# Performance work log

Hardware: AMD Instinct MI355X
Metric: run time of the kernel (lower is better)

## Reference

```python
import jax, jax.numpy as jnp
import numpy as np

N_FEAT = 350; D = 512; L = 4; DS = 64; NREG = 6; REG_E = 32
B = 32; S = 2048
CLAMP = 20.0


def _ln(x, g, b, eps=1e-5):
    mu = jnp.mean(x, axis=-1, keepdims=True)
    var = jnp.mean(jnp.square(x - mu), axis=-1, keepdims=True)
    return (x - mu) * jax.lax.rsqrt(var + eps) * g + b


def _slstm(x, ln_g, ln_b, Wi, bi, Wf, bf, Wz, bz, Wo, bo, Wp, bp):
    # x: [B,S,D] -> out: [B,S,D]
    xn = _ln(x, ln_g, ln_b)
    log_i = jnp.clip(jnp.einsum('bsd,de->bse', xn, Wi) + bi, -CLAMP, CLAMP)
    log_f = jnp.clip(jnp.einsum('bsd,de->bse', xn, Wf) + bf, -CLAMP, CLAMP)
    z = jnp.tanh(jnp.einsum('bsd,de->bse', xn, Wz) + bz)
    o = jax.nn.sigmoid(jnp.einsum('bsd,de->bse', xn, Wo) + bo)

    def step(carry, inp):
        m, c = carry
        li, lf, zt, ot = inp
        m_new = jnp.maximum(m + lf, li)
        i_s = jnp.exp(li - m_new)
        f_s = jnp.exp(m + lf - m_new)
        c_new = f_s * c + i_s * zt
        h = ot * jnp.tanh(c_new)
        return (m_new, c_new), h

    bsz = x.shape[0]
    init = (jnp.zeros((bsz, DS), x.dtype), jnp.zeros((bsz, DS), x.dtype))
    seq = (jnp.swapaxes(log_i, 0, 1), jnp.swapaxes(log_f, 0, 1),
           jnp.swapaxes(z, 0, 1), jnp.swapaxes(o, 0, 1))
    _, hs = jax.lax.scan(step, init, seq)  # hs: [S,B,DS]
    hs = jnp.swapaxes(hs, 0, 1)  # [B,S,DS]
    return jnp.einsum('bse,ed->bsd', hs, Wp) + bp


def setup_inputs() -> dict:
    key = jax.random.key(0)
    ks = iter(jax.random.split(key, 64))
    def p(*shape):
        return jax.random.normal(next(ks), shape, dtype=jnp.float32) * 0.02
    return {
        'x': jax.random.normal(next(ks), (B, S, N_FEAT), dtype=jnp.float32),
        'regime_ids': jax.random.randint(next(ks), (B, S), 0, NREG),
        'emb_regime': p(NREG, REG_E),
        'grn_w1': p(N_FEAT + REG_E, D), 'grn_b1': jnp.zeros((D,), jnp.float32),
        'grn_w2': p(D, N_FEAT), 'grn_b2': jnp.zeros((N_FEAT,), jnp.float32),
        'in_w': p(N_FEAT, D), 'in_b': jnp.zeros((D,), jnp.float32),
        'ln_in_g': jnp.ones((L, D), jnp.float32), 'ln_in_b': jnp.zeros((L, D), jnp.float32),
        'wi': p(L, D, DS), 'bi': jnp.zeros((L, DS), jnp.float32),
        'wf': p(L, D, DS), 'bf': jnp.zeros((L, DS), jnp.float32),
        'wz': p(L, D, DS), 'bz': jnp.zeros((L, DS), jnp.float32),
        'wo': p(L, D, DS), 'bo': jnp.zeros((L, DS), jnp.float32),
        'wp': p(L, DS, D), 'bp': jnp.zeros((L, D), jnp.float32),
        'nm_g': jnp.ones((L, D), jnp.float32), 'nm_b': jnp.zeros((L, D), jnp.float32),
        'hd15_w': p(D, 1), 'hd15_b': jnp.zeros((1,), jnp.float32),
        'hd30_w': p(D, 1), 'hd30_b': jnp.zeros((1,), jnp.float32),
        'hv_w': p(D, 3), 'hv_b': jnp.zeros((3,), jnp.float32),
        'hreg_w': p(D, NREG), 'hreg_b': jnp.zeros((NREG,), jnp.float32),
        'hrng_w': p(D, 3), 'hrng_b': jnp.zeros((3,), jnp.float32),
    }


def reference(x, regime_ids, emb_regime, grn_w1, grn_b1, grn_w2, grn_b2,
              in_w, in_b, ln_in_g, ln_in_b, wi, bi, wf, bf, wz, bz, wo, bo,
              wp, bp, nm_g, nm_b, hd15_w, hd15_b, hd30_w, hd30_b,
              hv_w, hv_b, hreg_w, hreg_b, hrng_w, hrng_b):
    # Variable selection network (regime-conditioned feature weights)
    remb = emb_regime[regime_ids]                      # [B,S,32]
    comb = jnp.concatenate([x, remb], axis=-1)         # [B,S,382]
    hidden = jax.nn.elu(jnp.einsum('bsf,fd->bsd', comb, grn_w1) + grn_b1)
    weights = jax.nn.softmax(jnp.einsum('bsd,df->bsf', hidden, grn_w2) + grn_b2, axis=-1)
    xw = x * weights
    h = jnp.einsum('bsf,fd->bsd', xw, in_w) + in_b     # [B,S,D]
    for l in range(L):
        res = _slstm(h, ln_in_g[l], ln_in_b[l], wi[l], bi[l], wf[l], bf[l],
                     wz[l], bz[l], wo[l], bo[l], wp[l], bp[l])
        h = _ln(h + res, nm_g[l], nm_b[l])
    h_last = h[:, -1, :]
    return (jnp.squeeze(h_last @ hd15_w + hd15_b, -1),
            jnp.squeeze(h_last @ hd30_w + hd30_b, -1),
            h_last @ hv_w + hv_b,
            h_last @ hreg_w + hreg_b,
            h_last @ hrng_w + hrng_b,
            h_last,
            weights[:, -1, :])
```

## Files before the change

kernel.cpp:

```cpp
#include <hip/hip_runtime.h>
#include <cmath>

#define NFEAT 350
#define DMODEL 512
#define NLAYER 4
#define DSZ 64
#define REG_E 32
#define BATCH 32
#define SEQ 2048
#define MTOK (BATCH * SEQ)
#define CLAMP_V 20.0f

#define CHUNK 64
#define NCHUNK (SEQ / CHUNK)

typedef short bf16x8 __attribute__((ext_vector_type(8)));
typedef float f32x4 __attribute__((ext_vector_type(4)));

__device__ __forceinline__ unsigned short f2b(float v) {
    union { float f; unsigned int u; } x; x.f = v;
    unsigned int r = x.u + 0x7fffu + ((x.u >> 16) & 1u);
    return (unsigned short)(r >> 16);
}
__device__ __forceinline__ float b2f(unsigned short u) {
    union { unsigned int i; float f; } x; x.i = ((unsigned int)u) << 16;
    return x.f;
}
__device__ __forceinline__ unsigned int pack2(float a, float b) {
    return ((unsigned int)f2b(b) << 16) | f2b(a);
}

__global__ __launch_bounds__(256) void tconv_k(const float* __restrict__ src,
                                               unsigned short* __restrict__ dst,
                                               int K, int N, int Kpad) {
    int k = blockIdx.x * 256 + threadIdx.x;
    int n = blockIdx.y;
    if (k >= Kpad) return;
    float v = (k < K && n < N) ? src[(size_t)k * N + n] : 0.f;
    dst[(size_t)n * Kpad + k] = f2b(v);
}

__global__ __launch_bounds__(256) void tconv_wp_k(const float* __restrict__ wp,
                                                  unsigned short* __restrict__ dst) {
    int idx = blockIdx.x * 256 + threadIdx.x;
    int l = idx >> 15;
    int rem = idx & 32767;
    int n = rem >> 6;
    int k = rem & 63;
    float v = wp[((size_t)l * 64 + k) * 512 + n];
    unsigned short hi = f2b(v);
    unsigned short lo = f2b(v - b2f(hi));
    unsigned short* d = dst + ((size_t)l * 512 + n) * 128;
    d[k] = hi;
    d[64 + k] = lo;
}

__global__ __launch_bounds__(256) void tconv_g_k(const float* __restrict__ wi,
                                                 const float* __restrict__ wf,
                                                 const float* __restrict__ wz,
                                                 const float* __restrict__ wo,
                                                 unsigned short* __restrict__ dst) {
    int k = blockIdx.x * 256 + threadIdx.x;
    int n = blockIdx.y;
    int z = blockIdx.z;
    int l = z >> 2, g = z & 3;
    const float* src = (g == 0 ? wi : g == 1 ? wf : g == 2 ? wz : wo) + (size_t)l * DMODEL * DSZ;
    dst[(size_t)z * 32768 + (size_t)n * 512 + k] = f2b(src[(size_t)k * DSZ + n]);
}

__global__ __launch_bounds__(1024) void gbias_k(const float* bi, const float* bf_,
                                                const float* bz, const float* bo,
                                                float* __restrict__ gbias) {
    int t = threadIdx.x;
    int l = t >> 8, r = t & 255, g = r >> 6, e = r & 63;
    const float* s = (g == 0 ? bi : g == 1 ? bf_ : g == 2 ? bz : bo);
    gbias[t] = s[l * 64 + e];
}

__global__ __launch_bounds__(256) void build_xc_k(const float* __restrict__ x,
                                                  const int* __restrict__ rid,
                                                  const float* __restrict__ emb,
                                                  unsigned short* __restrict__ xc) {
    int i = blockIdx.x * 256 + threadIdx.x;
    int m = i / 192, p = i - m * 192;
    int k = p * 2;
    float a = 0.f, b = 0.f;
    if (k < 350) {
        const float2 v = *(const float2*)(x + (size_t)m * NFEAT + k);
        a = v.x; b = v.y;
    } else if (k < 382) {
        int r = rid[m];
        const float2 v = *(const float2*)(emb + r * REG_E + (k - 350));
        a = v.x; b = v.y;
    }
    ((unsigned int*)xc)[(size_t)m * 192 + p] = pack2(a, b);
}

template <int ALD, int EPI>
__global__ __launch_bounds__(256) void mgemm_k(const unsigned short* __restrict__ Ab,
                                               const float* __restrict__ Af,
                                               const unsigned short* __restrict__ Bt,
                                               const float* __restrict__ bias,
                                               float* __restrict__ Cf,
                                               unsigned short* __restrict__ Cb,
                                               const float* __restrict__ muA,
                                               const float* __restrict__ rstdA,
                                               const float* __restrict__ lng,
                                               const float* __restrict__ lnb,
                                               int lda, int ldb, int K, int N, int ldc) {
    __shared__ unsigned short As[128][40];
    __shared__ unsigned short Bs[128][40];
    const int tid = threadIdx.x;
    const int lane = tid & 63;
    const int wave = tid >> 6;
    const int l15 = lane & 15;
    const int quad = lane >> 4;
    const int wm = (wave >> 1) * 64;
    const int wn = (wave & 1) * 64;
    const size_t m0 = (size_t)blockIdx.y * 128;
    const int n0 = blockIdx.x * 128;

    const int sr = tid >> 2;
    const int ku = tid & 3;

    const unsigned short* Br0 = Bt + ((size_t)(n0 + sr)) * ldb + ku * 8;
    const unsigned short* Br1 = Br0 + (size_t)64 * ldb;

    const unsigned short* Ar0 = nullptr;
    const unsigned short* Ar1 = nullptr;
    const float* Fr0 = nullptr;
    const float* Fr1 = nullptr;
    float mu0 = 0.f, rs0 = 0.f, mu1 = 0.f, rs1 = 0.f;
    if (ALD == 0) {
        Ar0 = Ab + (m0 + sr) * (size_t)lda + ku * 8;
        Ar1 = Ar0 + (size_t)64 * lda;
    } else {
        Fr0 = Af + (m0 + sr) * (size_t)lda + ku * 8;
        Fr1 = Fr0 + (size_t)64 * lda;
        mu0 = muA[m0 + sr];   rs0 = rstdA[m0 + sr];
        mu1 = muA[m0 + sr + 64]; rs1 = rstdA[m0 + sr + 64];
    }

    f32x4 acc[4][4] = {};

    for (int k0 = 0; k0 < K; k0 += 32) {
        if (ALD == 0) {
            *(uint4*)&As[sr][ku * 8]      = *(const uint4*)(Ar0 + k0);
            *(uint4*)&As[sr + 64][ku * 8] = *(const uint4*)(Ar1 + k0);
        } else {
            float4 g0 = *(const float4*)(lng + k0 + ku * 8);
            float4 g1 = *(const float4*)(lng + k0 + ku * 8 + 4);
            float4 c0 = *(const float4*)(lnb + k0 + ku * 8);
            float4 c1 = *(const float4*)(lnb + k0 + ku * 8 + 4);
            {
                float4 v0 = *(const float4*)(Fr0 + k0);
                float4 v1 = *(const float4*)(Fr0 + k0 + 4);
                uint4 w;
                w.x = pack2((v0.x - mu0) * rs0 * g0.x + c0.x, (v0.y - mu0) * rs0 * g0.y + c0.y);
                w.y = pack2((v0.z - mu0) * rs0 * g0.z + c0.z, (v0.w - mu0) * rs0 * g0.w + c0.w);
                w.z = pack2((v1.x - mu0) * rs0 * g1.x + c1.x, (v1.y - mu0) * rs0 * g1.y + c1.y);
                w.w = pack2((v1.z - mu0) * rs0 * g1.z + c1.z, (v1.w - mu0) * rs0 * g1.w + c1.w);
                *(uint4*)&As[sr][ku * 8] = w;
            }
            {
                float4 v0 = *(const float4*)(Fr1 + k0);
                float4 v1 = *(const float4*)(Fr1 + k0 + 4);
                uint4 w;
                w.x = pack2((v0.x - mu1) * rs1 * g0.x + c0.x, (v0.y - mu1) * rs1 * g0.y + c0.y);
                w.y = pack2((v0.z - mu1) * rs1 * g0.z + c0.z, (v0.w - mu1) * rs1 * g0.w + c0.w);
                w.z = pack2((v1.x - mu1) * rs1 * g1.x + c1.x, (v1.y - mu1) * rs1 * g1.y + c1.y);
                w.w = pack2((v1.z - mu1) * rs1 * g1.z + c1.z, (v1.w - mu1) * rs1 * g1.w + c1.w);
                *(uint4*)&As[sr + 64][ku * 8] = w;
            }
        }
        *(uint4*)&Bs[sr][ku * 8]      = *(const uint4*)(Br0 + k0);
        *(uint4*)&Bs[sr + 64][ku * 8] = *(const uint4*)(Br1 + k0);
        __syncthreads();
        bf16x8 af[4], bf[4];
#pragma unroll
        for (int mt = 0; mt < 4; mt++)
            af[mt] = *(const bf16x8*)&As[wm + mt * 16 + l15][quad * 8];
#pragma unroll
        for (int nt = 0; nt < 4; nt++)
            bf[nt] = *(const bf16x8*)&Bs[wn + nt * 16 + l15][quad * 8];
#pragma unroll
        for (int mt = 0; mt < 4; mt++)
#pragma unroll
            for (int nt = 0; nt < 4; nt++)
                acc[mt][nt] = __builtin_amdgcn_mfma_f32_16x16x32_bf16(af[mt], bf[nt], acc[mt][nt], 0, 0, 0);
        __syncthreads();
    }

#pragma unroll
    for (int mt = 0; mt < 4; mt++) {
        int gmb = wm + mt * 16 + quad * 4;
#pragma unroll
        for (int nt = 0; nt < 4; nt++) {
            int gn = n0 + wn + nt * 16 + l15;
            if (gn < N) {
                float bv = bias[gn];
#pragma unroll
                for (int r = 0; r < 4; r++) {
                    size_t gm = m0 + gmb + r;
                    float v = acc[mt][nt][r] + bv;
                    if (EPI == 0) {
                        v = v > 0.f ? v : expm1f(v);
                        Cb[gm * (size_t)ldc + gn] = f2b(v);
                    } else if (EPI == 1) {
                        Cb[gm * (size_t)ldc + gn] = f2b(v);
                    } else if (EPI == 2) {
                        int g = gn >> 6;
                        if (g < 2) v = fminf(fmaxf(v, -CLAMP_V), CLAMP_V);
                        else if (g == 2) v = tanhf(v);
                        else v = 1.f / (1.f + expf(-v));
                        Cf[gm * (size_t)ldc + gn] = v;
                    } else {
                        Cf[gm * (size_t)ldc + gn] = v;
                    }
                }
            }
        }
    }
}

__global__ __launch_bounds__(256) void softmax_xw_k(const unsigned short* __restrict__ logits,
                                                    unsigned short* __restrict__ xc,
                                                    float* __restrict__ out_wlast) {
    int tok = blockIdx.x * 4 + (threadIdx.x >> 6);
    int lane = threadIdx.x & 63;
    const unsigned short* lr = logits + (size_t)tok * NFEAT;
    unsigned short* xr = xc + (size_t)tok * 384;
    float v[6];
    float mx = -1e30f;
#pragma unroll
    for (int i = 0; i < 6; i++) {
        int idx = lane + 64 * i;
        v[i] = (idx < NFEAT) ? b2f(lr[idx]) : -1e30f;
        mx = fmaxf(mx, v[i]);
    }
#pragma unroll
    for (int o = 32; o > 0; o >>= 1) mx = fmaxf(mx, __shfl_xor(mx, o, 64));
    float s = 0.f;
#pragma unroll
    for (int i = 0; i < 6; i++) { v[i] = expf(v[i] - mx); s += v[i]; }
#pragma unroll
    for (int o = 32; o > 0; o >>= 1) s += __shfl_xor(s, o, 64);
    float inv = 1.f / s;
    bool last = ((tok & (SEQ - 1)) == SEQ - 1);
    int b = tok >> 11;
#pragma unroll
    for (int i = 0; i < 6; i++) {
        int idx = lane + 64 * i;
        if (idx < NFEAT) {
            float w = v[i] * inv;
            xr[idx] = f2b(w * b2f(xr[idx]));
            if (last) out_wlast[b * NFEAT + idx] = w;
        } else if (idx < 352) {
            xr[idx] = 0;
        }
    }
}

__global__ __launch_bounds__(256) void ln_stats_k(const float* __restrict__ h,
                                                  float* __restrict__ mu,
                                                  float* __restrict__ rstd) {
    int tok = blockIdx.x * 4 + (threadIdx.x >> 6);
    int lane = threadIdx.x & 63;
    const float* row = h + (size_t)tok * DMODEL;
    float s = 0.f, sq = 0.f;
#pragma unroll
    for (int i = 0; i < 8; i++) {
        float v = row[lane + 64 * i];
        s += v;
        sq += v * v;
    }
#pragma unroll
    for (int o = 32; o > 0; o >>= 1) {
        s += __shfl_xor(s, o, 64);
        sq += __shfl_xor(sq, o, 64);
    }
    if (lane == 0) {
        float m = s * (1.f / DMODEL);
        float var = sq * (1.f / DMODEL) - m * m;
        mu[tok] = m;
        rstd[tok] = rsqrtf(var + 1e-5f);
    }
}

__global__ __launch_bounds__(256) void seg_agg_k(const float* __restrict__ gates,
                                                 float* __restrict__ aggF,
                                                 float* __restrict__ aggL,
                                                 float* __restrict__ aggS) {
    int b = blockIdx.x >> 3;
    int cg = blockIdx.x & 7;
    int chunk = cg * 4 + (threadIdx.x >> 6);
    int e = threadIdx.x & 63;
    const float* gp = gates + ((size_t)b * SEQ + (size_t)chunk * CHUNK) * 256;
    float F = 0.f, L = -1e30f, s = 0.f;
#pragma unroll 4
    for (int t = 0; t < CHUNK; t++) {
        const float* q = gp + (size_t)t * 256;
        float li = q[e], lf = q[64 + e], z = q[128 + e];
        float Ln = fmaxf(L + lf, li);
        s = expf(L + lf - Ln) * s + expf(li - Ln) * z;
        L = Ln;
        F += lf;
    }
    int idx = (b * NCHUNK + chunk) * 64 + e;
    aggF[idx] = F; aggL[idx] = L; aggS[idx] = s;
}

__global__ __launch_bounds__(64) void chunk_scan_k(const float* __restrict__ aggF,
                                                   const float* __restrict__ aggL,
                                                   const float* __restrict__ aggS,
                                                   float* __restrict__ stM,
                                                   float* __restrict__ stC) {
    int b = blockIdx.x;
    int e = threadIdx.x;
    float m = 0.f, c = 0.f;
    for (int k = 0; k < NCHUNK; k++) {
        int idx = (b * NCHUNK + k) * 64 + e;
        stM[idx] = m; stC[idx] = c;
        float F = aggF[idx], L = aggL[idx], s = aggS[idx];
        float mn = fmaxf(m + F, L);
        c = expf(m + F - mn) * c + expf(L - mn) * s;
        m = mn;
    }
}

__global__ __launch_bounds__(256) void replay_k(const float* __restrict__ gates,
                                                const float* __restrict__ stM,
                                                const float* __restrict__ stC,
                                                unsigned short* __restrict__ hs) {
    int b = blockIdx.x >> 3;
    int cg = blockIdx.x & 7;
    int chunk = cg * 4 + (threadIdx.x >> 6);
    int e = threadIdx.x & 63;
    int s0 = chunk * CHUNK;
    const float* gp = gates + ((size_t)b * SEQ + s0) * 256;
    unsigned short* hp = hs + ((size_t)b * SEQ + s0) * 128;
    int idx = (b * NCHUNK + chunk) * 64 + e;
    float m = stM[idx], c = stC[idx];
#pragma unroll 4
    for (int t = 0; t < CHUNK; t++) {
        const float* q = gp + (size_t)t * 256;
        float li = q[e], lf = q[64 + e], z = q[128 + e], o = q[192 + e];
        float mlf = m + lf;
        float mn = fmaxf(mlf, li);
        c = expf(mlf - mn) * c + expf(li - mn) * z;
        m = mn;
        float v = o * tanhf(c);
        unsigned short hi = f2b(v);
        hp[(size_t)t * 128 + e] = hi;
        hp[(size_t)t * 128 + 64 + e] = f2b(v - b2f(hi));
    }
}

__global__ __launch_bounds__(512) void outproj_mfma_k(const unsigned short* __restrict__ hs,
                                                      const unsigned short* __restrict__ wpt,
                                                      const float* __restrict__ bp,
                                                      const float* __restrict__ nmg,
                                                      const float* __restrict__ nmb,
                                                      float* __restrict__ h,
                                                      float* __restrict__ mu,
                                                      float* __restrict__ rstd) {
    __shared__ unsigned short As[32][136];
    __shared__ float sS[32][4], sQ[32][4];
    __shared__ float sS2[32][4], sQ2[32][4];
    const int tid = threadIdx.x;
    const int lane = tid & 63;
    const int wave = tid >> 6;
    const int l15 = lane & 15;
    const int quad = lane >> 4;
    const int wm = (wave >> 2) * 16;
    const int wn = (wave & 3) * 128;
    const int cg = wave & 3;
    const size_t tok0 = (size_t)blockIdx.x * 32;

    {
        int row = tid >> 4, ku = tid & 15;
        *(uint4*)&As[row][ku * 8] = *(const uint4*)(hs + (tok0 + row) * 128 + ku * 8);
    }
    __syncthreads();

    f32x4 acc[8] = {};
#pragma unroll 1
    for (int term = 0; term < 3; term++) {
        const int aoff = (term == 2) ? 64 : 0;
        const int boff = (term == 1) ? 64 : 0;
#pragma unroll
        for (int ks = 0; ks < 2; ks++) {
            bf16x8 af = *(const bf16x8*)&As[wm + l15][aoff + ks * 32 + quad * 8];
#pragma unroll
            for (int nt = 0; nt < 8; nt++) {
                bf16x8 bv = *(const bf16x8*)(wpt + (size_t)(wn + nt * 16 + l15) * 128 + boff + ks * 32 + quad * 8);
                acc[nt] = __builtin_amdgcn_mfma_f32_16x16x32_bf16(af, bv, acc[nt], 0, 0, 0);
            }
        }
    }

    float bpv[8], gv[8], bv_[8];
#pragma unroll
    for (int nt = 0; nt < 8; nt++) {
        int col = wn + nt * 16 + l15;
        bpv[nt] = bp[col]; gv[nt] = nmg[col]; bv_[nt] = nmb[col];
    }

#pragma unroll
    for (int r = 0; r < 4; r++) {
        int trow = wm + quad * 4 + r;
        const float* hrow = h + (tok0 + trow) * (size_t)DMODEL;
        float s = 0.f, sq = 0.f;
#pragma unroll
        for (int nt = 0; nt < 8; nt++) {
            float u = acc[nt][r] + bpv[nt] + hrow[wn + nt * 16 + l15];
            acc[nt][r] = u;
            s += u; sq += u * u;
        }
#pragma unroll
        for (int o = 8; o > 0; o >>= 1) { s += __shfl_xor(s, o, 64); sq += __shfl_xor(sq, o, 64); }
        if (l15 == 0) { sS[trow][cg] = s; sQ[trow][cg] = sq; }
    }
    __syncthreads();

#pragma unroll
    for (int r = 0; r < 4; r++) {
        int trow = wm + quad * 4 + r;
        float s = sS[trow][0] + sS[trow][1] + sS[trow][2] + sS[trow][3];
        float sq = sQ[trow][0] + sQ[trow][1] + sQ[trow][2] + sQ[trow][3];
        float mean = s * (1.f / DMODEL);
        float var = sq * (1.f / DMODEL) - mean * mean;
        float rs = rsqrtf(var + 1e-5f);
        float* hrow = h + (tok0 + trow) * (size_t)DMODEL;
        float s2 = 0.f, sq2 = 0.f;
#pragma unroll
        for (int nt = 0; nt < 8; nt++) {
            float v = (acc[nt][r] - mean) * rs * gv[nt] + bv_[nt];
            hrow[wn + nt * 16 + l15] = v;
            s2 += v; sq2 += v * v;
        }
#pragma unroll
        for (int o = 8; o > 0; o >>= 1) { s2 += __shfl_xor(s2, o, 64); sq2 += __shfl_xor(sq2, o, 64); }
        if (l15 == 0) { sS2[trow][cg] = s2; sQ2[trow][cg] = sq2; }
    }
    __syncthreads();
    if (tid < 32) {
        float s2 = sS2[tid][0] + sS2[tid][1] + sS2[tid][2] + sS2[tid][3];
        float sq2 = sQ2[tid][0] + sQ2[tid][1] + sQ2[tid][2] + sQ2[tid][3];
        float m2 = s2 * (1.f / DMODEL);
        float v2 = sq2 * (1.f / DMODEL) - m2 * m2;
        mu[tok0 + tid] = m2;
        rstd[tok0 + tid] = rsqrtf(v2 + 1e-5f);
    }
}

__global__ __launch_bounds__(64) void heads_k(const float* __restrict__ h,
                                              const float* hd15_w, const float* hd15_b,
                                              const float* hd30_w, const float* hd30_b,
                                              const float* hv_w, const float* hv_b,
                                              const float* hreg_w, const float* hreg_b,
                                              const float* hrng_w, const float* hrng_b,
                                              float* __restrict__ out) {
    int b = blockIdx.x;
    int lane = threadIdx.x;
    __shared__ float row[DMODEL];
    const float* hp = h + (size_t)(b * SEQ + SEQ - 1) * DMODEL;
#pragma unroll
    for (int i = 0; i < 8; i++) row[lane + 64 * i] = hp[lane + 64 * i];
    __syncthreads();
#pragma unroll
    for (int i = 0; i < 8; i++) out[448 + b * DMODEL + lane + 64 * i] = row[lane + 64 * i];
    if (lane < 14) {
        const float* w; const float* bb;
        int ncol, j, off;
        if (lane == 0)      { w = hd15_w; bb = hd15_b; ncol = 1; j = 0;         off = 0 + b; }
        else if (lane == 1) { w = hd30_w; bb = hd30_b; ncol = 1; j = 0;         off = 32 + b; }
        else if (lane < 5)  { j = lane - 2;  w = hv_w;   bb = hv_b;   ncol = 3; off = 64 + b * 3 + j; }
        else if (lane < 11) { j = lane - 5;  w = hreg_w; bb = hreg_b; ncol = 6; off = 160 + b * 6 + j; }
        else                { j = lane - 11; w = hrng_w; bb = hrng_b; ncol = 3; off = 352 + b * 3 + j; }
        float s = bb[j];
        for (int k = 0; k < DMODEL; k++) s += row[k] * w[k * ncol + j];
        out[off] = s;
    }
}

extern "C" void kernel_launch(void* const* d_in, const int* in_sizes, int n_in,
                              void* d_out, int out_size, void* d_ws, size_t ws_size,
                              hipStream_t stream) {
    (void)in_sizes; (void)n_in; (void)out_size; (void)ws_size;
    const float* x      = (const float*)d_in[0];
    const int*   rid    = (const int*)d_in[1];
    const float* emb    = (const float*)d_in[2];
    const float* grn_w1 = (const float*)d_in[3];
    const float* grn_b1 = (const float*)d_in[4];
    const float* grn_w2 = (const float*)d_in[5];
    const float* grn_b2 = (const float*)d_in[6];
    const float* in_w   = (const float*)d_in[7];
    const float* in_b   = (const float*)d_in[8];
    const float* ln_g   = (const float*)d_in[9];
    const float* ln_b   = (const float*)d_in[10];
    const float* wi     = (const float*)d_in[11];
    const float* bi     = (const float*)d_in[12];
    const float* wf     = (const float*)d_in[13];
    const float* bf_    = (const float*)d_in[14];
    const float* wz     = (const float*)d_in[15];
    const float* bz     = (const float*)d_in[16];
    const float* wo     = (const float*)d_in[17];
    const float* bo     = (const float*)d_in[18];
    const float* wp     = (const float*)d_in[19];
    const float* bp     = (const float*)d_in[20];
    const float* nm_g   = (const float*)d_in[21];
    const float* nm_b   = (const float*)d_in[22];

    float* out = (float*)d_out;
    char* W = (char*)d_ws;

    float* h               = (float*)W;
    unsigned short* hidden = (unsigned short*)W;
    unsigned short* logits = (unsigned short*)(W + 67108864);
    char* RB = W + 134217728;
    unsigned short* xc = (unsigned short*)RB;
    float* gates  = (float*)RB;
    unsigned short* hsbuf = (unsigned short*)(RB + 67108864);
    char* RM = W + 218103808;
    float* aggF  = (float*)(RM);
    float* aggL  = (float*)(RM + 262144);
    float* aggS  = (float*)(RM + 524288);
    float* stM   = (float*)(RM + 786432);
    float* stC   = (float*)(RM + 1048576);
    float* mu    = (float*)(RM + 1310720);
    float* rstd  = (float*)(RM + 1572864);
    unsigned short* w1t  = (unsigned short*)(RM + 1835008);
    unsigned short* w2t  = (unsigned short*)(RM + 2228224);
    unsigned short* inwt = (unsigned short*)(RM + 2621440);
    unsigned short* gwt  = (unsigned short*)(RM + 2981888);
    float* gbias         = (float*)(RM + 4030464);
    unsigned short* wpt  = (unsigned short*)(RM + 4034560);

    build_xc_k<<<MTOK * 192 / 256, 256, 0, stream>>>(x, rid, emb, xc);
    tconv_k<<<dim3(2, 512), 256, 0, stream>>>(grn_w1, w1t, 382, 512, 384);
    tconv_k<<<dim3(2, 384), 256, 0, stream>>>(grn_w2, w2t, 512, 350, 512);
    tconv_k<<<dim3(2, 512), 256, 0, stream>>>(in_w, inwt, 350, 512, 352);
    tconv_g_k<<<dim3(2, 64, 16), 256, 0, stream>>>(wi, wf, wz, wo, gwt);
    gbias_k<<<1, 1024, 0, stream>>>(bi, bf_, bz, bo, gbias);
    tconv_wp_k<<<512, 256, 0, stream>>>(wp, wpt);

    mgemm_k<0, 0><<<dim3(4, 512), 256, 0, stream>>>(xc, nullptr, w1t, grn_b1, nullptr, hidden,
                                                    nullptr, nullptr, nullptr, nullptr,
                                                    384, 384, 384, 512, 512);
    mgemm_k<0, 1><<<dim3(3, 512), 256, 0, stream>>>(hidden, nullptr, w2t, grn_b2, nullptr, logits,
                                                    nullptr, nullptr, nullptr, nullptr,
                                                    512, 512, 512, 350, 350);
    softmax_xw_k<<<MTOK / 4, 256, 0, stream>>>(logits, xc, out + 16832);
    mgemm_k<0, 3><<<dim3(4, 512), 256, 0, stream>>>(xc, nullptr, inwt, in_b, h, nullptr,
                                                    nullptr, nullptr, nullptr, nullptr,
                                                    384, 352, 352, 512, 512);
    ln_stats_k<<<MTOK / 4, 256, 0, stream>>>(h, mu, rstd);

    for (int l = 0; l < NLAYER; l++) {
        mgemm_k<1, 2><<<dim3(2, 512), 256, 0, stream>>>(nullptr, h, gwt + (size_t)l * 131072,
                                                        gbias + l * 256, gates, nullptr,
                                                        mu, rstd,
                                                        ln_g + l * DMODEL, ln_b + l * DMODEL,
                                                        512, 512, 512, 256, 256);
        seg_agg_k<<<BATCH * 8, 256, 0, stream>>>(gates, aggF, aggL, aggS);
        chunk_scan_k<<<BATCH, 64, 0, stream>>>(aggF, aggL, aggS, stM, stC);
        replay_k<<<BATCH * 8, 256, 0, stream>>>(gates, stM, stC, hsbuf);

        outproj_mfma_k<<<MTOK / 32, 512, 0, stream>>>(hsbuf,
                                                      wpt + (size_t)l * 65536,
                                                      bp + l * DMODEL,
                                                      nm_g + l * DMODEL,
                                                      nm_b + l * DMODEL,
                                                      h, mu, rstd);
    }

    heads_k<<<BATCH, 64, 0, stream>>>(h,
                                      (const float*)d_in[23], (const float*)d_in[24],
                                      (const float*)d_in[25], (const float*)d_in[26],
                                      (const float*)d_in[27], (const float*)d_in[28],
                                      (const float*)d_in[29], (const float*)d_in[30],
                                      (const float*)d_in[31], (const float*)d_in[32],
                                      out);
}
```

Measured before the change: 1.510 ms.

## Restructure outproj kernel to 16-token tiles with LDS-staged row-wise LayerNorm

```diff
diff --git a/kernel.cpp b/kernel.cpp
--- a/kernel.cpp
+++ b/kernel.cpp
@@ -356,7 +356,7 @@
     }
 }
 
-__global__ __launch_bounds__(512) void outproj_mfma_k(const unsigned short* __restrict__ hs,
+__global__ __launch_bounds__(256) void outproj_mfma_k(const unsigned short* __restrict__ hs,
                                                       const unsigned short* __restrict__ wpt,
                                                       const float* __restrict__ bp,
                                                       const float* __restrict__ nmg,
@@ -364,18 +364,22 @@
                                                       float* __restrict__ h,
                                                       float* __restrict__ mu,
                                                       float* __restrict__ rstd) {
-    __shared__ unsigned short As[32][136];
-    __shared__ float sS[32][4], sQ[32][4];
-    __shared__ float sS2[32][4], sQ2[32][4];
+    __shared__ unsigned short As[16][168];
+    __shared__ float proj[16][520];
     const int tid = threadIdx.x;
     const int lane = tid & 63;
-    const int wave = tid >> 6;
+    const int wv = tid >> 6;
     const int l15 = lane & 15;
     const int quad = lane >> 4;
-    const int wm = (wave >> 2) * 16;
-    const int wn = (wave & 3) * 128;
-    const int cg = wave & 3;
-    const size_t tok0 = (size_t)blockIdx.x * 32;
+    const int wn = wv * 128;
+    const size_t tok0 = (size_t)blockIdx.x * 16;
+
+    float bpv[8], gv[8], bv_[8];
+#pragma unroll
+    for (int j = 0; j < 8; j++) {
+        int col = lane + 64 * j;
+        bpv[j] = bp[col]; gv[j] = nmg[col]; bv_[j] = nmb[col];
+    }
 
     {
         int row = tid >> 4, ku = tid & 15;
@@ -383,74 +387,78 @@
     }
     __syncthreads();
 
+    bf16x8 a_hi0 = *(const bf16x8*)&As[l15][quad * 8];
+    bf16x8 a_hi1 = *(const bf16x8*)&As[l15][32 + quad * 8];
+    bf16x8 a_lo0 = *(const bf16x8*)&As[l15][64 + quad * 8];
+    bf16x8 a_lo1 = *(const bf16x8*)&As[l15][96 + quad * 8];
+
     f32x4 acc[8] = {};
 #pragma unroll 1
     for (int term = 0; term < 3; term++) {
-        const int aoff = (term == 2) ? 64 : 0;
+        const bf16x8 af0 = (term == 2) ? a_lo0 : a_hi0;
+        const bf16x8 af1 = (term == 2) ? a_lo1 : a_hi1;
         const int boff = (term == 1) ? 64 : 0;
-#pragma unroll
-        for (int ks = 0; ks < 2; ks++) {
-            bf16x8 af = *(const bf16x8*)&As[wm + l15][aoff + ks * 32 + quad * 8];
-#pragma unroll
-            for (int nt = 0; nt < 8; nt++) {
-                bf16x8 bv = *(const bf16x8*)(wpt + (size_t)(wn + nt * 16 + l15) * 128 + boff + ks * 32 + quad * 8);
-                acc[nt] = __builtin_amdgcn_mfma_f32_16x16x32_bf16(af, bv, acc[nt], 0, 0, 0);
-            }
+        bf16x8 bv[2][8];
+#pragma unroll
+        for (int ks = 0; ks < 2; ks++)
+#pragma unroll
+            for (int nt = 0; nt < 8; nt++)
+                bv[ks][nt] = *(const bf16x8*)(wpt + (size_t)(wn + nt * 16 + l15) * 128 + boff + ks * 32 + quad * 8);
+#pragma unroll
+        for (int nt = 0; nt < 8; nt++)
+            acc[nt] = __builtin_amdgcn_mfma_f32_16x16x32_bf16(af0, bv[0][nt], acc[nt], 0, 0, 0);
+#pragma unroll
+        for (int nt = 0; nt < 8; nt++)
+            acc[nt] = __builtin_amdgcn_mfma_f32_16x16x32_bf16(af1, bv[1][nt], acc[nt], 0, 0, 0);
+    }
+
+    float hv[4][8];
+#pragma unroll
+    for (int t = 0; t < 4; t++)
+#pragma unroll
+        for (int j = 0; j < 8; j++)
+            hv[t][j] = h[(tok0 + wv * 4 + t) * (size_t)DMODEL + lane + 64 * j];
+
+#pragma unroll
+    for (int nt = 0; nt < 8; nt++)
+#pragma unroll
+        for (int r = 0; r < 4; r++)
+            proj[quad * 4 + r][wn + nt * 16 + l15] = acc[nt][r];
+    __syncthreads();
+
+#pragma unroll
+    for (int t = 0; t < 4; t++) {
+        int trow = wv * 4 + t;
+        size_t tok = tok0 + trow;
+        float u[8];
+        float s = 0.f, sq = 0.f;
+#pragma unroll
+        for (int j = 0; j < 8; j++) {
+            float v = hv[t][j] + proj[trow][lane + 64 * j] + bpv[j];
+            u[j] = v;
+            s += v; sq += v * v;
         }
-    }
-
-    float bpv[8], gv[8], bv_[8];
-#pragma unroll
-    for (int nt = 0; nt < 8; nt++) {
-        int col = wn + nt * 16 + l15;
-        bpv[nt] = bp[col]; gv[nt] = nmg[col]; bv_[nt] = nmb[col];
-    }
-
-#pragma unroll
-    for (int r = 0; r < 4; r++) {
-        int trow = wm + quad * 4 + r;
-        const float* hrow = h + (tok0 + trow) * (size_t)DMODEL;
-        float s = 0.f, sq = 0.f;
-#pragma unroll
-        for (int nt = 0; nt < 8; nt++) {
-            float u = acc[nt][r] + bpv[nt] + hrow[wn + nt * 16 + l15];
-            acc[nt][r] = u;
-            s += u; sq += u * u;
-        }
-#pragma unroll
-        for (int o = 8; o > 0; o >>= 1) { s += __shfl_xor(s, o, 64); sq += __shfl_xor(sq, o, 64); }
-        if (l15 == 0) { sS[trow][cg] = s; sQ[trow][cg] = sq; }
-    }
-    __syncthreads();
-
-#pragma unroll
-    for (int r = 0; r < 4; r++) {
-        int trow = wm + quad * 4 + r;
-        float s = sS[trow][0] + sS[trow][1] + sS[trow][2] + sS[trow][3];
-        float sq = sQ[trow][0] + sQ[trow][1] + sQ[trow][2] + sQ[trow][3];
+#pragma unroll
+        for (int o = 32; o > 0; o >>= 1) { s += __shfl_xor(s, o, 64); sq += __shfl_xor(sq, o, 64); }
         float mean = s * (1.f / DMODEL);
         float var = sq * (1.f / DMODEL) - mean * mean;
         float rs = rsqrtf(var + 1e-5f);
-        float* hrow = h + (tok0 + trow) * (size_t)DMODEL;
+        float* hrow = h + tok * (size_t)DMODEL;
         float s2 = 0.f, sq2 = 0.f;
 #pragma unroll
-        for (int nt = 0; nt < 8; nt++) {
-            float v = (acc[nt][r] - mean) * rs * gv[nt] + bv_[nt];
-            hrow[wn + nt * 16 + l15] = v;
+        for (int j = 0; j < 8; j++) {
+            float v = (u[j] - mean) * rs * gv[j] + bv_[j];
+            hrow[lane + 64 * j] = v;
             s2 += v; sq2 += v * v;
         }
 #pragma unroll
-        for (int o = 8; o > 0; o >>= 1) { s2 += __shfl_xor(s2, o, 64); sq2 += __shfl_xor(sq2, o, 64); }
-        if (l15 == 0) { sS2[trow][cg] = s2; sQ2[trow][cg] = sq2; }
-    }
-    __syncthreads();
-    if (tid < 32) {
-        float s2 = sS2[tid][0] + sS2[tid][1] + sS2[tid][2] + sS2[tid][3];
-        float sq2 = sQ2[tid][0] + sQ2[tid][1] + sQ2[tid][2] + sQ2[tid][3];
-        float m2 = s2 * (1.f / DMODEL);
-        float v2 = sq2 * (1.f / DMODEL) - m2 * m2;
-        mu[tok0 + tid] = m2;
-        rstd[tok0 + tid] = rsqrtf(v2 + 1e-5f);
+        for (int o = 32; o > 0; o >>= 1) { s2 += __shfl_xor(s2, o, 64); sq2 += __shfl_xor(sq2, o, 64); }
+        if (lane == 0) {
+            float m2 = s2 * (1.f / DMODEL);
+            float v2 = sq2 * (1.f / DMODEL) - m2 * m2;
+            mu[tok] = m2;
+            rstd[tok] = rsqrtf(v2 + 1e-5f);
+        }
     }
 }
 
@@ -567,7 +575,7 @@
         chunk_scan_k<<<BATCH, 64, 0, stream>>>(aggF, aggL, aggS, stM, stC);
         replay_k<<<BATCH * 8, 256, 0, stream>>>(gates, stM, stC, hsbuf);
 
-        outproj_mfma_k<<<MTOK / 32, 512, 0, stream>>>(hsbuf,
+        outproj_mfma_k<<<MTOK / 16, 256, 0, stream>>>(hsbuf,
                                                       wpt + (size_t)l * 65536,
                                                       bp + l * DMODEL,
                                                       nm_g + l * DMODEL,
```

Measured after the change: 1.415 ms. 1.07x faster.

## Restructure output projection so each wave owns full token rows, recomputing GEMM

Applied to the files above, without the earlier changes.

```diff
diff --git a/kernel.cpp b/kernel.cpp
--- a/kernel.cpp
+++ b/kernel.cpp
@@ -364,93 +364,122 @@
                                                       float* __restrict__ h,
                                                       float* __restrict__ mu,
                                                       float* __restrict__ rstd) {
-    __shared__ unsigned short As[32][136];
-    __shared__ float sS[32][4], sQ[32][4];
-    __shared__ float sS2[32][4], sQ2[32][4];
     const int tid = threadIdx.x;
     const int lane = tid & 63;
-    const int wave = tid >> 6;
+    const int wv = tid >> 6;
     const int l15 = lane & 15;
     const int quad = lane >> 4;
-    const int wm = (wave >> 2) * 16;
-    const int wn = (wave & 3) * 128;
-    const int cg = wave & 3;
-    const size_t tok0 = (size_t)blockIdx.x * 32;
-
-    {
-        int row = tid >> 4, ku = tid & 15;
-        *(uint4*)&As[row][ku * 8] = *(const uint4*)(hs + (tok0 + row) * 128 + ku * 8);
-    }
-    __syncthreads();
-
-    f32x4 acc[8] = {};
+    const size_t tok0 = (size_t)blockIdx.x * 128 + wv * 16;
+
+    const unsigned short* ar = hs + (tok0 + l15) * 128;
+    bf16x8 a_hi0 = *(const bf16x8*)(ar + quad * 8);
+    bf16x8 a_hi1 = *(const bf16x8*)(ar + 32 + quad * 8);
+    bf16x8 a_lo0 = *(const bf16x8*)(ar + 64 + quad * 8);
+    bf16x8 a_lo1 = *(const bf16x8*)(ar + 96 + quad * 8);
+
+    const float* hbase = h + (tok0 + quad * 4) * (size_t)DMODEL;
+
+    float s1[4] = {0.f, 0.f, 0.f, 0.f}, q1[4] = {0.f, 0.f, 0.f, 0.f};
+
 #pragma unroll 1
-    for (int term = 0; term < 3; term++) {
-        const int aoff = (term == 2) ? 64 : 0;
-        const int boff = (term == 1) ? 64 : 0;
-#pragma unroll
-        for (int ks = 0; ks < 2; ks++) {
-            bf16x8 af = *(const bf16x8*)&As[wm + l15][aoff + ks * 32 + quad * 8];
-#pragma unroll
-            for (int nt = 0; nt < 8; nt++) {
-                bf16x8 bv = *(const bf16x8*)(wpt + (size_t)(wn + nt * 16 + l15) * 128 + boff + ks * 32 + quad * 8);
-                acc[nt] = __builtin_amdgcn_mfma_f32_16x16x32_bf16(af, bv, acc[nt], 0, 0, 0);
+    for (int cg = 0; cg < 4; cg++) {
+        f32x4 acc[8] = {};
+        const unsigned short* wb = wpt + (size_t)(cg * 128 + l15) * 128 + quad * 8;
+#pragma unroll 1
+        for (int term = 0; term < 3; term++) {
+            const bf16x8 af0 = (term == 2) ? a_lo0 : a_hi0;
+            const bf16x8 af1 = (term == 2) ? a_lo1 : a_hi1;
+            const int boff = (term == 1) ? 64 : 0;
+#pragma unroll
+            for (int ks = 0; ks < 2; ks++) {
+                const bf16x8 af = ks ? af1 : af0;
+#pragma unroll
+                for (int nt = 0; nt < 8; nt++) {
+                    bf16x8 bv = *(const bf16x8*)(wb + nt * 2048 + boff + ks * 32);
+                    acc[nt] = __builtin_amdgcn_mfma_f32_16x16x32_bf16(af, bv, acc[nt], 0, 0, 0);
+                }
             }
         }
-    }
-
-    float bpv[8], gv[8], bv_[8];
-#pragma unroll
-    for (int nt = 0; nt < 8; nt++) {
-        int col = wn + nt * 16 + l15;
-        bpv[nt] = bp[col]; gv[nt] = nmg[col]; bv_[nt] = nmb[col];
-    }
-
+#pragma unroll
+        for (int nt = 0; nt < 8; nt++) {
+            int col = cg * 128 + nt * 16 + l15;
+            float bpv = bp[col];
+#pragma unroll
+            for (int r = 0; r < 4; r++) {
+                float u = acc[nt][r] + bpv + hbase[(size_t)r * DMODEL + col];
+                s1[r] += u; q1[r] += u * u;
+            }
+        }
+    }
 #pragma unroll
     for (int r = 0; r < 4; r++) {
-        int trow = wm + quad * 4 + r;
-        const float* hrow = h + (tok0 + trow) * (size_t)DMODEL;
-        float s = 0.f, sq = 0.f;
+#pragma unroll
+        for (int o = 1; o < 16; o <<= 1) {
+            s1[r] += __shfl_xor(s1[r], o, 64);
+            q1[r] += __shfl_xor(q1[r], o, 64);
+        }
+    }
+    float mean[4], rs[4];
+#pragma unroll
+    for (int r = 0; r < 4; r++) {
+        mean[r] = s1[r] * (1.f / DMODEL);
+        float var = q1[r] * (1.f / DMODEL) - mean[r] * mean[r];
+        rs[r] = rsqrtf(var + 1e-5f);
+    }
+
+    float s2[4] = {0.f, 0.f, 0.f, 0.f}, q2[4] = {0.f, 0.f, 0.f, 0.f};
+    float* hwb = h + (tok0 + quad * 4) * (size_t)DMODEL;
+#pragma unroll 1
+    for (int cg = 0; cg < 4; cg++) {
+        f32x4 acc[8] = {};
+        const unsigned short* wb = wpt + (size_t)(cg * 128 + l15) * 128 + quad * 8;
+#pragma unroll 1
+        for (int term = 0; term < 3; term++) {
+            const bf16x8 af0 = (term == 2) ? a_lo0 : a_hi0;
+            const bf16x8 af1 = (term == 2) ? a_lo1 : a_hi1;
+            const int boff = (term == 1) ? 64 : 0;
+#pragma unroll
+            for (int ks = 0; ks < 2; ks++) {
+                const bf16x8 af = ks ? af1 : af0;
+#pragma unroll
+                for (int nt = 0; nt < 8; nt++) {
+                    bf16x8 bv = *(const bf16x8*)(wb + nt * 2048 + boff + ks * 32);
+                    acc[nt] = __builtin_amdgcn_mfma_f32_16x16x32_bf16(af, bv, acc[nt], 0, 0, 0);
+                }
+            }
+        }
 #pragma unroll
         for (int nt = 0; nt < 8; nt++) {
-            float u = acc[nt][r] + bpv[nt] + hrow[wn + nt * 16 + l15];
-            acc[nt][r] = u;
-            s += u; sq += u * u;
-        }
-#pragma unroll
-        for (int o = 8; o > 0; o >>= 1) { s += __shfl_xor(s, o, 64); sq += __shfl_xor(sq, o, 64); }
-        if (l15 == 0) { sS[trow][cg] = s; sQ[trow][cg] = sq; }
-    }
-    __syncthreads();
-
+            int col = cg * 128 + nt * 16 + l15;
+            float bpv = bp[col];
+            float gvv = nmg[col];
+            float bbv = nmb[col];
+#pragma unroll
+            for (int r = 0; r < 4; r++) {
+                float u = acc[nt][r] + bpv + hbase[(size_t)r * DMODEL + col];
+                float v = (u - mean[r]) * rs[r] * gvv + bbv;
+                hwb[(size_t)r * DMODEL + col] = v;
+                s2[r] += v; q2[r] += v * v;
+            }
+        }
+    }
 #pragma unroll
     for (int r = 0; r < 4; r++) {
-        int trow = wm + quad * 4 + r;
-        float s = sS[trow][0] + sS[trow][1] + sS[trow][2] + sS[trow][3];
-        float sq = sQ[trow][0] + sQ[trow][1] + sQ[trow][2] + sQ[trow][3];
-        float mean = s * (1.f / DMODEL);
-        float var = sq * (1.f / DMODEL) - mean * mean;
-        float rs = rsqrtf(var + 1e-5f);
-        float* hrow = h + (tok0 + trow) * (size_t)DMODEL;
-        float s2 = 0.f, sq2 = 0.f;
-#pragma unroll
-        for (int nt = 0; nt < 8; nt++) {
-            float v = (acc[nt][r] - mean) * rs * gv[nt] + bv_[nt];
-            hrow[wn + nt * 16 + l15] = v;
-            s2 += v; sq2 += v * v;
-        }
-#pragma unroll
-        for (int o = 8; o > 0; o >>= 1) { s2 += __shfl_xor(s2, o, 64); sq2 += __shfl_xor(sq2, o, 64); }
-        if (l15 == 0) { sS2[trow][cg] = s2; sQ2[trow][cg] = sq2; }
-    }
-    __syncthreads();
-    if (tid < 32) {
-        float s2 = sS2[tid][0] + sS2[tid][1] + sS2[tid][2] + sS2[tid][3];
-        float sq2 = sQ2[tid][0] + sQ2[tid][1] + sQ2[tid][2] + sQ2[tid][3];
-        float m2 = s2 * (1.f / DMODEL);
-        float v2 = sq2 * (1.f / DMODEL) - m2 * m2;
-        mu[tok0 + tid] = m2;
-        rstd[tok0 + tid] = rsqrtf(v2 + 1e-5f);
+#pragma unroll
+        for (int o = 1; o < 16; o <<= 1) {
+            s2[r] += __shfl_xor(s2[r], o, 64);
+            q2[r] += __shfl_xor(q2[r], o, 64);
+        }
+    }
+    if (l15 == 0) {
+#pragma unroll
+        for (int r = 0; r < 4; r++) {
+            size_t tok = tok0 + quad * 4 + r;
+            float m2 = s2[r] * (1.f / DMODEL);
+            float v2 = q2[r] * (1.f / DMODEL) - m2 * m2;
+            mu[tok] = m2;
+            rstd[tok] = rsqrtf(v2 + 1e-5f);
+        }
     }
 }
 
@@ -567,12 +596,12 @@
         chunk_scan_k<<<BATCH, 64, 0, stream>>>(aggF, aggL, aggS, stM, stC);
         replay_k<<<BATCH * 8, 256, 0, stream>>>(gates, stM, stC, hsbuf);
 
-        outproj_mfma_k<<<MTOK / 32, 512, 0, stream>>>(hsbuf,
-                                                      wpt + (size_t)l * 65536,
-                                                      bp + l * DMODEL,
-                                                      nm_g + l * DMODEL,
-                                                      nm_b + l * DMODEL,
-                                                      h, mu, rstd);
+        outproj_mfma_k<<<MTOK / 128, 512, 0, stream>>>(hsbuf,
+                                                       wpt + (size_t)l * 65536,
+                                                       bp + l * DMODEL,
+                                                       nm_g + l * DMODEL,
+                                                       nm_b + l * DMODEL,
+                                                       h, mu, rstd);
     }
 
     heads_k<<<BATCH, 64, 0, stream>>>(h,
```

Result: slower. 1.877 ms (+24.3%).
